# Optimization experiments

Measured on AMD Instinct MI355X. Metric: run time of the kernel, lower is better.

## Reference

```python
import jax, jax.numpy as jnp
import numpy as np

B, T, D, H, LORA = 4, 1024, 1024, 16, 64
HD = D // H
BLOCK_ID, N_BLOCKS = 6, 12


def _ln(x, w, b, eps=1e-5):
    m = x.mean(-1, keepdims=True)
    v = ((x - m) ** 2).mean(-1, keepdims=True)
    return (x - m) * jax.lax.rsqrt(v + eps) * w + b


def _lora(z, a, b, l):
    return l + jnp.tanh(z @ a.T) @ b.T


def setup_inputs() -> dict:
    key = jax.random.key(0)
    ks = iter(jax.random.split(key, 64))
    rn = lambda shape, s: jax.random.normal(next(ks), shape, jnp.float32) * s
    inp = {}
    inp['x'] = rn((B, T, D), 1.0)
    r1 = 1.0 - BLOCK_ID / N_BLOCKS
    i = np.arange(D)
    inp['xw'] = jnp.asarray(1.0 - (i / D) ** r1, jnp.float32)
    for nm in ('rW', 'kW', 'vW', 'gW'):
        inp[nm] = rn((D, D), 0.02)
    for p in ('r', 'k', 'v', 'g', 'd'):
        inp[p + '_la'] = rn((LORA, D), 0.001)
        inp[p + '_lb'] = rn((D, LORA), 0.001)
        inp[p + '_ll'] = rn((D,), 1.0)
    inp['ln_w'] = jnp.full((HD,), ((1 + BLOCK_ID) / N_BLOCKS) ** 0.7, jnp.float32)
    inp['ln_b'] = jnp.zeros((HD,), jnp.float32)
    inp['oW'] = rn((D, D), 0.02)
    inp['init_state'] = rn((H, HD, HD), 1.0)
    r0 = BLOCK_ID / (N_BLOCKS - 1)
    ih = i % HD
    inp['u'] = jnp.asarray(r0 * (1 - ih / (D - 1)) + np.remainder(0.1 * (ih + 1), 3.0), jnp.float32)
    return inp


def reference(x, xw, rW, kW, vW, gW, r_la, r_lb, r_ll, k_la, k_lb, k_ll,
              v_la, v_lb, v_ll, g_la, g_lb, g_ll, d_la, d_lb, d_ll,
              ln_w, ln_b, oW, init_state, u):
    b, t, d = x.shape
    h = init_state.shape[0]
    hd = d // h
    # token shift: xx[t] = x[t-1], xx[0] = 0
    xx = jnp.concatenate([jnp.zeros_like(x[:, :1]), x[:, :-1]], axis=1)
    dx = xx - x
    lerpx = x + dx * xw
    r = (x + dx * _lora(lerpx, r_la, r_lb, r_ll)) @ rW.T
    k = (x + dx * _lora(lerpx, k_la, k_lb, k_ll)) @ kW.T
    v = (x + dx * _lora(lerpx, v_la, v_lb, v_ll)) @ vW.T
    g = (x + dx * _lora(lerpx, g_la, g_lb, g_ll)) @ gW.T
    w = jnp.exp(-jnp.exp(_lora(x + dx * _lora(lerpx, d_la, d_lb, d_ll), d_la, d_lb, d_ll)))
    # [B,T,D] -> [T,B,H,hd] for the time scan
    split = lambda z: z.reshape(b, t, h, hd).transpose(1, 0, 2, 3)
    rs, ws, ks, vs = split(r), split(w), split(k), split(v)
    uh = u.reshape(h, hd)
    st0 = jnp.broadcast_to(init_state, (b, h, hd, hd))

    def step(st, inp):
        rt, wt, kt, vt = inp
        kv = jnp.einsum('bhi,bhj->bhij', kt, vt)      # outer product
        y = jnp.einsum('bhi,bhij->bhj', rt, st + uh[None, :, :, None] * kv)
        return wt[..., None] * st + kv, y             # diag(w) @ S + kv

    st1, ys = jax.lax.scan(step, st0, (rs, ws, ks, vs))  # ys: [T,B,H,hd]
    o = jax.nn.silu(g.reshape(b, t, h, hd)) * _ln(ys.transpose(1, 0, 2, 3), ln_w, ln_b)
    return o.reshape(b, t, d) @ oW.T, st1
```

## Files before the change

### kernel.cpp

```cpp
#include <hip/hip_runtime.h>
#include <hip/hip_bf16.h>

typedef unsigned short u16;
typedef unsigned int u32;
typedef __attribute__((ext_vector_type(4))) float f32x4;
typedef __attribute__((ext_vector_type(4))) u32 u32x4;
typedef __attribute__((ext_vector_type(8))) short s16x8;

#define AS1 __attribute__((address_space(1)))
#define AS3 __attribute__((address_space(3)))

#define NB 4
#define TTOK 1024
#define DD 1024
#define NH 16
#define HD 64
#define MT 4096
#define NCH 16
#define CLEN 64

static __device__ __forceinline__ float b2f(u16 u) {
  union { unsigned int u; float f; } c; c.u = ((unsigned int)u) << 16; return c.f;
}
static __device__ __forceinline__ float ubit(u32 u) {
  union { u32 u; float f; } c; c.u = u; return c.f;
}
static __device__ __forceinline__ u16 f2b(float f) {
  union { float f; unsigned int u; } c; c.f = f;
  return (u16)((c.u + 0x7fffu + ((c.u >> 16) & 1u)) >> 16);
}
static __device__ __forceinline__ void gload16(const u16* g, u16* l) {
  __builtin_amdgcn_global_load_lds((const AS1 u32*)g, (AS3 u32*)l, 16, 0, 0);
}
static __device__ __forceinline__ int swz(int lin) {
  return lin ^ (((lin >> 9) & 3) << 5) ^ (((lin >> 7) & 1) << 4);
}

__global__ __launch_bounds__(256) void convW(const float* __restrict__ s0, const float* __restrict__ s1,
                                             const float* __restrict__ s2, const float* __restrict__ s3,
                                             const float* __restrict__ s4, u16* __restrict__ dst) {
  long f = ((long)blockIdx.x * 256 + threadIdx.x) << 2;
  int sel = (int)(f >> 20);
  const float* s = sel == 0 ? s0 : sel == 1 ? s1 : sel == 2 ? s2 : sel == 3 ? s3 : s4;
  long off = f & 1048575;
  f32x4 v = *(const f32x4*)&s[off];
  ushort4 o; o.x = f2b(v[0]); o.y = f2b(v[1]); o.z = f2b(v[2]); o.w = f2b(v[3]);
  *(ushort4*)&dst[f] = o;
}

__global__ __launch_bounds__(256) void convLora(
    const float* a0, const float* a1, const float* a2, const float* a3, const float* a4,
    const float* b0, const float* b1, const float* b2, const float* b3, const float* b4,
    const float* l0, const float* l1, const float* l2, const float* l3, const float* l4,
    u16* __restrict__ laD, u16* __restrict__ lbD, float* __restrict__ llD) {
  long f = ((long)blockIdx.x * 256 + threadIdx.x) << 2;
  if (f < 327680) {
    int sel = (int)(f >> 16); long off = f & 65535;
    const float* s = sel == 0 ? a0 : sel == 1 ? a1 : sel == 2 ? a2 : sel == 3 ? a3 : a4;
    f32x4 v = *(const f32x4*)&s[off];
    ushort4 o; o.x = f2b(v[0]); o.y = f2b(v[1]); o.z = f2b(v[2]); o.w = f2b(v[3]);
    *(ushort4*)&laD[f] = o;
  } else if (f < 655360) {
    long g = f - 327680;
    int sel = (int)(g >> 16); long off = g & 65535;
    const float* s = sel == 0 ? b0 : sel == 1 ? b1 : sel == 2 ? b2 : sel == 3 ? b3 : b4;
    f32x4 v = *(const f32x4*)&s[off];
    ushort4 o; o.x = f2b(v[0]); o.y = f2b(v[1]); o.z = f2b(v[2]); o.w = f2b(v[3]);
    *(ushort4*)&lbD[g] = o;
  } else if (f < 660480) {
    long g = f - 655360;
    int sel = (int)(g >> 10); long off = g & 1023;
    const float* s = sel == 0 ? l0 : sel == 1 ? l1 : sel == 2 ? l2 : sel == 3 ? l3 : l4;
    *(f32x4*)&llD[g] = *(const f32x4*)&s[off];
  }
}

__global__ __launch_bounds__(256) void prep(const float* __restrict__ x, const float* __restrict__ xw,
                                            u16* __restrict__ lerpx, u16* __restrict__ xB,
                                            u16* __restrict__ dxB) {
  long f = ((long)blockIdx.x * 256 + threadIdx.x) << 2;
  int d = (int)(f & (DD - 1));
  int m = (int)(f >> 10);
  int t = m & (TTOK - 1);
  f32x4 xv = *(const f32x4*)&x[f];
  f32x4 xm = {};
  if (t > 0) xm = *(const f32x4*)&x[f - DD];
  f32x4 xwv = *(const f32x4*)&xw[d];
  f32x4 dx = xm - xv;
  f32x4 lp = xv + dx * xwv;
  ushort4 o; o.x = f2b(lp[0]); o.y = f2b(lp[1]); o.z = f2b(lp[2]); o.w = f2b(lp[3]);
  *(ushort4*)&lerpx[f] = o;
  ushort4 ox; ox.x = f2b(xv[0]); ox.y = f2b(xv[1]); ox.z = f2b(xv[2]); ox.w = f2b(xv[3]);
  *(ushort4*)&xB[f] = ox;
  ushort4 od; od.x = f2b(dx[0]); od.y = f2b(dx[1]); od.z = f2b(dx[2]); od.w = f2b(dx[3]);
  *(ushort4*)&dxB[f] = od;
}

template<int BM, int BN, int EPI>
__launch_bounds__(256)
__global__ void gemm2(const u16* __restrict__ Ab, long sAz,
                      const u16* __restrict__ Bb, long sBz,
                      void* __restrict__ Ob, long sOz,
                      const float* __restrict__ llb,
                      const u16* __restrict__ xB,
                      const u16* __restrict__ dxB,
                      int M, int N, int K) {
  __shared__ __align__(16) u16 As[BM * 64];
  __shared__ __align__(16) u16 Bs[BN * 64];
  const int z = blockIdx.z;
  const u16* A = Ab + (long)z * sAz;
  const u16* Bw = Bb + (long)z * sBz;
  const int m0 = blockIdx.y * BM;
  const int n0 = blockIdx.x * BN;
  const int tid = threadIdx.x;
  const int l = tid & 63;
  const int wv = tid >> 6;
  constexpr int WM = BM / 2, WN = BN / 2;
  constexpr int FM = WM / 16, FN = WN / 16;
  const int wm0 = (wv >> 1) * WM, wn0 = (wv & 1) * WN;
  const int lrow = l & 15, lk = (l >> 4) * 8;
  constexpr int GA = BM / 32, GB = BN / 32;
  int gA[GA], gB[GB];
#pragma unroll
  for (int q = 0; q < GA; ++q) {
    int d = (q * 256 + tid) * 16;
    int bb = swz(d);
    gA[q] = (m0 + (bb >> 7)) * K + ((bb & 127) >> 1);
  }
#pragma unroll
  for (int q = 0; q < GB; ++q) {
    int d = (q * 256 + tid) * 16;
    int bb = swz(d);
    gB[q] = (n0 + (bb >> 7)) * K + ((bb & 127) >> 1);
  }
  int aOff[FM][2], bOff[FN][2];
#pragma unroll
  for (int m = 0; m < FM; ++m)
#pragma unroll
    for (int kk = 0; kk < 2; ++kk)
      aOff[m][kk] = swz(((wm0 + m * 16 + lrow) << 7) + (kk << 6) + (lk << 1));
#pragma unroll
  for (int n = 0; n < FN; ++n)
#pragma unroll
    for (int kk = 0; kk < 2; ++kk)
      bOff[n][kk] = swz(((wn0 + n * 16 + lrow) << 7) + (kk << 6) + (lk << 1));
  f32x4 acc[FM][FN] = {};
  for (int k0 = 0; k0 < K; k0 += 64) {
    __syncthreads();
#pragma unroll
    for (int q = 0; q < GA; ++q)
      gload16(&A[(long)gA[q] + k0], (u16*)((char*)As + (q * 256 + tid) * 16));
#pragma unroll
    for (int q = 0; q < GB; ++q)
      gload16(&Bw[(long)gB[q] + k0], (u16*)((char*)Bs + (q * 256 + tid) * 16));
    __syncthreads();
#pragma unroll
    for (int kk = 0; kk < 2; ++kk) {
      s16x8 af[FM], bfr[FN];
#pragma unroll
      for (int m = 0; m < FM; ++m) af[m] = *(const s16x8*)((const char*)As + aOff[m][kk]);
#pragma unroll
      for (int n = 0; n < FN; ++n) bfr[n] = *(const s16x8*)((const char*)Bs + bOff[n][kk]);
#pragma unroll
      for (int m = 0; m < FM; ++m)
#pragma unroll
        for (int n = 0; n < FN; ++n)
          acc[m][n] = __builtin_amdgcn_mfma_f32_16x16x32_bf16(af[m], bfr[n], acc[m][n], 0, 0, 0);
    }
  }
#pragma unroll
  for (int m = 0; m < FM; ++m) {
#pragma unroll
    for (int n = 0; n < FN; ++n) {
      const int j = n0 + wn0 + n * 16 + lrow;
#pragma unroll
      for (int q = 0; q < 4; ++q) {
        const int i = m0 + wm0 + m * 16 + (l >> 4) * 4 + q;
        const long off = (long)i * N + j;
        float v = acc[m][n][q];
        if constexpr (EPI == 0) {
          ((float*)Ob + (long)z * sOz)[off] = v;
        } else if constexpr (EPI == 1) {
          ((u16*)Ob + (long)z * sOz)[off] = f2b(tanhf(v));
        } else if constexpr (EPI == 2) {
          float val = b2f(xB[off]) + b2f(dxB[off]) * (llb[(long)z * N + j] + v);
          ((u16*)Ob + (long)z * sOz)[off] = f2b(val);
        } else if constexpr (EPI == 3) {
          ((float*)Ob + (long)z * sOz)[off] = expf(-expf(llb[j] + v));
        } else {
          ((u16*)Ob + (long)z * sOz)[off] = f2b(v);
        }
      }
    }
  }
}

__global__ __launch_bounds__(256) void scan_local(
    const u16* __restrict__ rP, const u16* __restrict__ kP,
    const u16* __restrict__ vP, const float* __restrict__ wP,
    const float* __restrict__ uP,
    u16* __restrict__ ys0, u16* __restrict__ ys1,
    u16* __restrict__ ys2, u16* __restrict__ ys3,
    u16* __restrict__ rtil, float* __restrict__ SL, float* __restrict__ AC) {
  __shared__ __align__(16) u16 Rs[64 * 64];
  __shared__ __align__(16) u16 Ks[64 * 64];
  __shared__ __align__(16) u16 Vs[64 * 64];
  __shared__ __align__(16) float Ws[64 * 64];
  const int bhc = blockIdx.x;
  const int c = bhc & (NCH - 1), h = (bhc >> 4) & (NH - 1), b = bhc >> 8;
  const int tid = threadIdx.x;
  const int j = tid & 63;
  const int qu = tid >> 6;
  const long base0 = ((long)(b * TTOK + c * CLEN) << 10) + h * HD;
#pragma unroll
  for (int q = 0; q < 2; ++q) {
    int cidx = q * 256 + tid;
    int t = cidx >> 3, off = (cidx & 7) * 8;
    gload16(&rP[base0 + (long)t * DD + off], (u16*)Rs + cidx * 8);
    gload16(&kP[base0 + (long)t * DD + off], (u16*)Ks + cidx * 8);
    gload16(&vP[base0 + (long)t * DD + off], (u16*)Vs + cidx * 8);
  }
#pragma unroll
  for (int q = 0; q < 4; ++q) {
    int cidx = q * 256 + tid;
    int t = cidx >> 4, off = (cidx & 15) * 4;
    __builtin_amdgcn_global_load_lds((const AS1 u32*)&wP[base0 + (long)t * DD + off],
                                     (AS3 u32*)((float*)Ws + cidx * 4), 16, 0, 0);
  }
  __syncthreads();
  const int so = qu * 16;
  float s[16];
#pragma unroll
  for (int x = 0; x < 16; ++x) s[x] = 0.f;
  float Aj = 1.f;
  const float uj = uP[h * HD + j];
  long base = base0;
  u16* __restrict__ ysel = qu == 0 ? ys0 : qu == 1 ? ys1 : qu == 2 ? ys2 : ys3;
  for (int tt = 0; tt < CLEN; ++tt) {
    const int ro = tt * 64 + so;
    u32x4 ra = *(const u32x4*)&Rs[ro];
    u32x4 rb = *(const u32x4*)&Rs[ro + 8];
    u32x4 ka = *(const u32x4*)&Ks[ro];
    u32x4 kb = *(const u32x4*)&Ks[ro + 8];
    float wl[16];
#pragma unroll
    for (int e = 0; e < 4; ++e) *(f32x4*)&wl[e * 4] = *(const f32x4*)&Ws[ro + e * 4];
    const float vj = b2f(Vs[tt * 64 + j]);
    float ya = 0.f, yb = 0.f;
#pragma unroll
    for (int e = 0; e < 4; ++e) {
      const float r0 = ubit(ra[e] << 16), r1 = ubit(ra[e] & 0xffff0000u);
      const float k0 = ubit(ka[e] << 16), k1 = ubit(ka[e] & 0xffff0000u);
      ya = fmaf(r0, s[2 * e], ya);
      s[2 * e] = fmaf(wl[2 * e], s[2 * e], k0 * vj);
      yb = fmaf(r1, s[2 * e + 1], yb);
      s[2 * e + 1] = fmaf(wl[2 * e + 1], s[2 * e + 1], k1 * vj);
    }
#pragma unroll
    for (int e = 0; e < 4; ++e) {
      const float r0 = ubit(rb[e] << 16), r1 = ubit(rb[e] & 0xffff0000u);
      const float k0 = ubit(kb[e] << 16), k1 = ubit(kb[e] & 0xffff0000u);
      ya = fmaf(r0, s[8 + 2 * e], ya);
      s[8 + 2 * e] = fmaf(wl[8 + 2 * e], s[8 + 2 * e], k0 * vj);
      yb = fmaf(r1, s[8 + 2 * e + 1], yb);
      s[8 + 2 * e + 1] = fmaf(wl[8 + 2 * e + 1], s[8 + 2 * e + 1], k1 * vj);
    }
    float y = ya + yb;
    if (qu == 0) {
      const float rj = b2f(Rs[tt * 64 + j]);
      const float kj = b2f(Ks[tt * 64 + j]);
      const float wj = Ws[tt * 64 + j];
      rtil[base + j] = f2b(rj * Aj);
      float al = rj * uj * kj;
#pragma unroll
      for (int msk = 1; msk < 64; msk <<= 1) al += __shfl_xor(al, msk, 64);
      y = fmaf(al, vj, y);
      Aj *= wj;
    }
    ysel[base + j] = f2b(y);
    base += DD;
  }
#pragma unroll
  for (int x = 0; x < 16; ++x)
    SL[((long)bhc * 64 + so + x) * 64 + j] = s[x];
  if (qu == 0) AC[(long)bhc * 64 + j] = Aj;
}

__global__ __launch_bounds__(256) void scan_prop(
    float* __restrict__ SL, const float* __restrict__ AC,
    const float* __restrict__ initS, float* __restrict__ st1) {
  const int bh = blockIdx.x >> 2;
  const int jq = blockIdx.x & 3;
  const int h = bh & (NH - 1);
  const int i = threadIdx.x >> 2;
  const int jo = jq * 16 + (threadIdx.x & 3) * 4;
  f32x4 sin4 = *(const f32x4*)(initS + ((long)h * 64 + i) * 64 + jo);
  for (int cc = 0; cc < NCH; ++cc) {
    const long bhc = (long)bh * NCH + cc;
    f32x4* slp = (f32x4*)(SL + (bhc * 64 + i) * 64 + jo);
    const float Ai = AC[bhc * 64 + i];
    f32x4 sl = *slp;
    *slp = sin4;
    sin4 = Ai * sin4 + sl;
  }
  *(f32x4*)(st1 + ((long)bh * 64 + i) * 64 + jo) = sin4;
}

__global__ __launch_bounds__(256) void scan_corr(
    const float* __restrict__ SL, const u16* __restrict__ rtil, float* __restrict__ ysC) {
  __shared__ __align__(16) float S[64 * 64];
  const int bhc = blockIdx.x;
  const int c = bhc & (NCH - 1), h = (bhc >> 4) & (NH - 1), b = bhc >> 8;
  const int tid = threadIdx.x;
  const f32x4* sp = (const f32x4*)(SL + (long)bhc * 4096);
  for (int q = tid; q < 1024; q += 256) ((f32x4*)S)[q] = sp[q];
  __syncthreads();
  const int t = tid >> 2, jg = (tid & 3) * 16;
  const long base = ((long)(b * TTOK + c * CLEN + t) * DD) + h * HD;
  f32x4 yacc[4] = {};
  const u16* rp = rtil + base;
#pragma unroll 8
  for (int i = 0; i < 64; ++i) {
    const float r = b2f(rp[i]);
    const f32x4* srow = (const f32x4*)&S[i * 64 + jg];
#pragma unroll
    for (int e = 0; e < 4; ++e) yacc[e] += r * srow[e];
  }
  f32x4* yp = (f32x4*)(ysC + base + jg);
#pragma unroll
  for (int e = 0; e < 4; ++e) yp[e] = yacc[e];
}

__global__ __launch_bounds__(256) void ln_silu(
    const u16* __restrict__ p0, const u16* __restrict__ p1,
    const u16* __restrict__ p2, const u16* __restrict__ p3,
    const float* __restrict__ ysC,
    const u16* __restrict__ gP,
    const float* __restrict__ lnw, const float* __restrict__ lnb,
    u16* __restrict__ oB) {
  const int ridx = blockIdx.x * 4 + (threadIdx.x >> 6);
  const int lane = threadIdx.x & 63;
  const long basem = (long)ridx * 64;
  const float y = b2f(p0[basem + lane]) + b2f(p1[basem + lane]) +
                  b2f(p2[basem + lane]) + b2f(p3[basem + lane]) + ysC[basem + lane];
  float su = y, sq = y * y;
#pragma unroll
  for (int msk = 1; msk < 64; msk <<= 1) {
    su += __shfl_xor(su, msk, 64);
    sq += __shfl_xor(sq, msk, 64);
  }
  const float mean = su * (1.f / 64.f);
  const float var = sq * (1.f / 64.f) - mean * mean;
  const float rs = rsqrtf(var + 1e-5f);
  const float g = b2f(gP[basem + lane]);
  const float silu = g / (1.f + expf(-g));
  const float val = silu * ((y - mean) * rs * lnw[lane] + lnb[lane]);
  oB[basem + lane] = f2b(val);
}

extern "C" void kernel_launch(void* const* d_in, const int* in_sizes, int n_in,
                              void* d_out, int out_size, void* d_ws, size_t ws_size,
                              hipStream_t stream) {
  const float* x   = (const float*)d_in[0];
  const float* xw  = (const float*)d_in[1];
  const float* rW  = (const float*)d_in[2];
  const float* kW  = (const float*)d_in[3];
  const float* vW  = (const float*)d_in[4];
  const float* gW  = (const float*)d_in[5];
  const float* r_la = (const float*)d_in[6],  *r_lb = (const float*)d_in[7],  *r_ll = (const float*)d_in[8];
  const float* k_la = (const float*)d_in[9],  *k_lb = (const float*)d_in[10], *k_ll = (const float*)d_in[11];
  const float* v_la = (const float*)d_in[12], *v_lb = (const float*)d_in[13], *v_ll = (const float*)d_in[14];
  const float* g_la = (const float*)d_in[15], *g_lb = (const float*)d_in[16], *g_ll = (const float*)d_in[17];
  const float* d_la = (const float*)d_in[18], *d_lb = (const float*)d_in[19], *d_ll = (const float*)d_in[20];
  const float* lnw = (const float*)d_in[21];
  const float* lnb = (const float*)d_in[22];
  const float* oW  = (const float*)d_in[23];
  const float* initS = (const float*)d_in[24];
  const float* uP  = (const float*)d_in[25];
  float* out = (float*)d_out;

  char* ws = (char*)d_ws;
  u16*   W_all  = (u16*)(ws + 0);
  u16*   la_all = (u16*)(ws + 10485760);
  u16*   lb_all = (u16*)(ws + 11141120);
  float* ll_all = (float*)(ws + 11796480);
  u16*   lerpx  = (u16*)(ws + 11816960);
  u16*   xB     = (u16*)(ws + 20205568);
  u16*   dxB    = (u16*)(ws + 28594176);
  u16*   t1_all = (u16*)(ws + 36982784);
  u16*   z_all  = (u16*)(ws + 39604224);
  u16*   rkvg   = (u16*)(ws + 81547264);
  float* wbuf   = (float*)(ws + 115101696);
  u16*   rtil   = (u16*)(ws + 131878912);
  float* SL     = (float*)(ws + 140267520);
  float* AC     = (float*)(ws + 157044736);
  u16*   ys0p   = (u16*)(ws + 157306880);
  u16*   oB     = (u16*)(ws + 174084096);
  u16*   ys1p   = (u16*)(ws + 11816960);
  u16*   ys2p   = (u16*)(ws + 39604224);
  u16*   ys3p   = (u16*)(ws + 47992832);
  float* ysC    = (float*)(ws + 115101696);

  convW<<<5120, 256, 0, stream>>>(rW, kW, vW, gW, oW, W_all);
  convLora<<<645, 256, 0, stream>>>(r_la, k_la, v_la, g_la, d_la,
                                    r_lb, k_lb, v_lb, g_lb, d_lb,
                                    r_ll, k_ll, v_ll, g_ll, d_ll,
                                    la_all, lb_all, ll_all);
  prep<<<4096, 256, 0, stream>>>(x, xw, lerpx, xB, dxB);

  gemm2<64, 64, 1><<<dim3(1, 64, 5), 256, 0, stream>>>(
      lerpx, 0L, la_all, 65536L, (void*)t1_all, 262144L, nullptr, nullptr, nullptr, MT, 64, 1024);
  gemm2<128, 128, 2><<<dim3(8, 32, 5), 256, 0, stream>>>(
      t1_all, 262144L, lb_all, 65536L, (void*)z_all, 4194304L, ll_all, xB, dxB, MT, 1024, 64);
  gemm2<64, 64, 1><<<dim3(1, 64, 1), 256, 0, stream>>>(
      z_all + 4L * 4194304, 0L, la_all + 4L * 65536, 0L, (void*)t1_all, 0L, nullptr, nullptr, nullptr, MT, 64, 1024);
  gemm2<128, 128, 3><<<dim3(8, 32, 1), 256, 0, stream>>>(
      t1_all, 0L, lb_all + 4L * 65536, 0L, (void*)wbuf, 0L, ll_all + 4096, nullptr, nullptr, MT, 1024, 64);
  gemm2<128, 128, 4><<<dim3(8, 32, 4), 256, 0, stream>>>(
      z_all, 4194304L, W_all, 1048576L, (void*)rkvg, 4194304L, nullptr, nullptr, nullptr, MT, 1024, 1024);

  scan_local<<<1024, 256, 0, stream>>>(rkvg, rkvg + 4194304L, rkvg + 2L * 4194304, wbuf,
                                       uP, ys0p, ys1p, ys2p, ys3p, rtil, SL, AC);
  scan_prop<<<256, 256, 0, stream>>>(SL, AC, initS, out + 4194304);
  scan_corr<<<1024, 256, 0, stream>>>(SL, rtil, ysC);

  ln_silu<<<16384, 256, 0, stream>>>(ys0p, ys1p, ys2p, ys3p, ysC, rkvg + 3L * 4194304, lnw, lnb, oB);
  gemm2<128, 128, 0><<<dim3(8, 32, 1), 256, 0, stream>>>(
      oB, 0L, W_all + 4L * 1048576, 0L, (void*)out, 0L, nullptr, nullptr, nullptr, MT, 1024, 1024);
}
```

Measured before the change: 368.4 us.

## Split scan state rows across 8 waves with packed FMA and swap GEMM grid order

The chunk-local scan now runs 512 threads per block, so each wave holds 8 state rows instead of 16. Its inner loop uses two-wide float vector FMAs, and the rtil and bonus-term work moves onto two different waves. Partial y outputs grow from four buffers to eight, and ln_silu sums all eight. GEMM block indexing is also swapped so the M tiles vary along blockIdx.x, which changes tile scheduling order. Serial per-block latency should fall, at the cost of more partial-output traffic and extra workspace aliasing.

```diff
diff --git a/kernel.cpp b/kernel.cpp
--- a/kernel.cpp
+++ b/kernel.cpp
@@ -3,6 +3,7 @@
 
 typedef unsigned short u16;
 typedef unsigned int u32;
+typedef __attribute__((ext_vector_type(2))) float f32x2;
 typedef __attribute__((ext_vector_type(4))) float f32x4;
 typedef __attribute__((ext_vector_type(4))) u32 u32x4;
 typedef __attribute__((ext_vector_type(8))) short s16x8;
@@ -18,6 +19,9 @@
 #define MT 4096
 #define NCH 16
 #define CLEN 64
+
+struct Ptr8 { u16* p[8]; };
+struct CPtr8 { const u16* p[8]; };
 
 static __device__ __forceinline__ float b2f(u16 u) {
   union { unsigned int u; float f; } c; c.u = ((unsigned int)u) << 16; return c.f;
@@ -110,8 +114,8 @@
   const int z = blockIdx.z;
   const u16* A = Ab + (long)z * sAz;
   const u16* Bw = Bb + (long)z * sBz;
-  const int m0 = blockIdx.y * BM;
-  const int n0 = blockIdx.x * BN;
+  const int m0 = blockIdx.x * BM;
+  const int n0 = blockIdx.y * BN;
   const int tid = threadIdx.x;
   const int l = tid & 63;
   const int wv = tid >> 6;
@@ -195,12 +199,10 @@
   }
 }
 
-__global__ __launch_bounds__(256) void scan_local(
+__global__ __launch_bounds__(512) void scan_local(
     const u16* __restrict__ rP, const u16* __restrict__ kP,
     const u16* __restrict__ vP, const float* __restrict__ wP,
-    const float* __restrict__ uP,
-    u16* __restrict__ ys0, u16* __restrict__ ys1,
-    u16* __restrict__ ys2, u16* __restrict__ ys3,
+    const float* __restrict__ uP, Ptr8 YS,
     u16* __restrict__ rtil, float* __restrict__ SL, float* __restrict__ AC) {
   __shared__ __align__(16) u16 Rs[64 * 64];
   __shared__ __align__(16) u16 Ks[64 * 64];
@@ -212,77 +214,68 @@
   const int j = tid & 63;
   const int qu = tid >> 6;
   const long base0 = ((long)(b * TTOK + c * CLEN) << 10) + h * HD;
+  {
+    int t = tid >> 3, off = (tid & 7) * 8;
+    gload16(&rP[base0 + (long)t * DD + off], (u16*)Rs + tid * 8);
+    gload16(&kP[base0 + (long)t * DD + off], (u16*)Ks + tid * 8);
+    gload16(&vP[base0 + (long)t * DD + off], (u16*)Vs + tid * 8);
+  }
 #pragma unroll
   for (int q = 0; q < 2; ++q) {
-    int cidx = q * 256 + tid;
-    int t = cidx >> 3, off = (cidx & 7) * 8;
-    gload16(&rP[base0 + (long)t * DD + off], (u16*)Rs + cidx * 8);
-    gload16(&kP[base0 + (long)t * DD + off], (u16*)Ks + cidx * 8);
-    gload16(&vP[base0 + (long)t * DD + off], (u16*)Vs + cidx * 8);
-  }
-#pragma unroll
-  for (int q = 0; q < 4; ++q) {
-    int cidx = q * 256 + tid;
+    int cidx = q * 512 + tid;
     int t = cidx >> 4, off = (cidx & 15) * 4;
     __builtin_amdgcn_global_load_lds((const AS1 u32*)&wP[base0 + (long)t * DD + off],
                                      (AS3 u32*)((float*)Ws + cidx * 4), 16, 0, 0);
   }
   __syncthreads();
-  const int so = qu * 16;
-  float s[16];
-#pragma unroll
-  for (int x = 0; x < 16; ++x) s[x] = 0.f;
+  const int so = qu * 8;
+  f32x2 s2[4] = {};
   float Aj = 1.f;
-  const float uj = uP[h * HD + j];
+  const float uj = (qu == 1) ? uP[h * HD + j] : 0.f;
   long base = base0;
-  u16* __restrict__ ysel = qu == 0 ? ys0 : qu == 1 ? ys1 : qu == 2 ? ys2 : ys3;
+  u16* __restrict__ ysel =
+      qu == 0 ? YS.p[0] : qu == 1 ? YS.p[1] : qu == 2 ? YS.p[2] : qu == 3 ? YS.p[3] :
+      qu == 4 ? YS.p[4] : qu == 5 ? YS.p[5] : qu == 6 ? YS.p[6] : YS.p[7];
   for (int tt = 0; tt < CLEN; ++tt) {
     const int ro = tt * 64 + so;
     u32x4 ra = *(const u32x4*)&Rs[ro];
-    u32x4 rb = *(const u32x4*)&Rs[ro + 8];
     u32x4 ka = *(const u32x4*)&Ks[ro];
-    u32x4 kb = *(const u32x4*)&Ks[ro + 8];
-    float wl[16];
-#pragma unroll
-    for (int e = 0; e < 4; ++e) *(f32x4*)&wl[e * 4] = *(const f32x4*)&Ws[ro + e * 4];
+    f32x2 wv2[4];
+#pragma unroll
+    for (int e = 0; e < 4; ++e) wv2[e] = *(const f32x2*)&Ws[ro + 2 * e];
     const float vj = b2f(Vs[tt * 64 + j]);
-    float ya = 0.f, yb = 0.f;
+    const f32x2 vj2 = {vj, vj};
+    f32x2 y2 = {0.f, 0.f};
 #pragma unroll
     for (int e = 0; e < 4; ++e) {
-      const float r0 = ubit(ra[e] << 16), r1 = ubit(ra[e] & 0xffff0000u);
-      const float k0 = ubit(ka[e] << 16), k1 = ubit(ka[e] & 0xffff0000u);
-      ya = fmaf(r0, s[2 * e], ya);
-      s[2 * e] = fmaf(wl[2 * e], s[2 * e], k0 * vj);
-      yb = fmaf(r1, s[2 * e + 1], yb);
-      s[2 * e + 1] = fmaf(wl[2 * e + 1], s[2 * e + 1], k1 * vj);
+      const u32 pr = ra[e], pk = ka[e];
+      f32x2 r01; r01[0] = ubit(pr << 16); r01[1] = ubit(pr & 0xffff0000u);
+      f32x2 k01; k01[0] = ubit(pk << 16); k01[1] = ubit(pk & 0xffff0000u);
+      y2 = __builtin_elementwise_fma(r01, s2[e], y2);
+      s2[e] = __builtin_elementwise_fma(wv2[e], s2[e], k01 * vj2);
     }
-#pragma unroll
-    for (int e = 0; e < 4; ++e) {
-      const float r0 = ubit(rb[e] << 16), r1 = ubit(rb[e] & 0xffff0000u);
-      const float k0 = ubit(kb[e] << 16), k1 = ubit(kb[e] & 0xffff0000u);
-      ya = fmaf(r0, s[8 + 2 * e], ya);
-      s[8 + 2 * e] = fmaf(wl[8 + 2 * e], s[8 + 2 * e], k0 * vj);
-      yb = fmaf(r1, s[8 + 2 * e + 1], yb);
-      s[8 + 2 * e + 1] = fmaf(wl[8 + 2 * e + 1], s[8 + 2 * e + 1], k1 * vj);
-    }
-    float y = ya + yb;
+    float y = y2[0] + y2[1];
     if (qu == 0) {
       const float rj = b2f(Rs[tt * 64 + j]);
-      const float kj = b2f(Ks[tt * 64 + j]);
       const float wj = Ws[tt * 64 + j];
       rtil[base + j] = f2b(rj * Aj);
+      Aj *= wj;
+    } else if (qu == 1) {
+      const float rj = b2f(Rs[tt * 64 + j]);
+      const float kj = b2f(Ks[tt * 64 + j]);
       float al = rj * uj * kj;
 #pragma unroll
       for (int msk = 1; msk < 64; msk <<= 1) al += __shfl_xor(al, msk, 64);
       y = fmaf(al, vj, y);
-      Aj *= wj;
     }
     ysel[base + j] = f2b(y);
     base += DD;
   }
 #pragma unroll
-  for (int x = 0; x < 16; ++x)
-    SL[((long)bhc * 64 + so + x) * 64 + j] = s[x];
+  for (int e = 0; e < 4; ++e) {
+    SL[((long)bhc * 64 + so + 2 * e) * 64 + j] = s2[e][0];
+    SL[((long)bhc * 64 + so + 2 * e + 1) * 64 + j] = s2[e][1];
+  }
   if (qu == 0) AC[(long)bhc * 64 + j] = Aj;
 }
 
@@ -332,17 +325,16 @@
 }
 
 __global__ __launch_bounds__(256) void ln_silu(
-    const u16* __restrict__ p0, const u16* __restrict__ p1,
-    const u16* __restrict__ p2, const u16* __restrict__ p3,
-    const float* __restrict__ ysC,
+    CPtr8 P, const float* __restrict__ ysC,
     const u16* __restrict__ gP,
     const float* __restrict__ lnw, const float* __restrict__ lnb,
     u16* __restrict__ oB) {
   const int ridx = blockIdx.x * 4 + (threadIdx.x >> 6);
   const int lane = threadIdx.x & 63;
   const long basem = (long)ridx * 64;
-  const float y = b2f(p0[basem + lane]) + b2f(p1[basem + lane]) +
-                  b2f(p2[basem + lane]) + b2f(p3[basem + lane]) + ysC[basem + lane];
+  float y = ysC[basem + lane];
+#pragma unroll
+  for (int q = 0; q < 8; ++q) y += b2f(P.p[q][basem + lane]);
   float su = y, sq = y * y;
 #pragma unroll
   for (int msk = 1; msk < 64; msk <<= 1) {
@@ -396,10 +388,17 @@
   float* AC     = (float*)(ws + 157044736);
   u16*   ys0p   = (u16*)(ws + 157306880);
   u16*   oB     = (u16*)(ws + 174084096);
-  u16*   ys1p   = (u16*)(ws + 11816960);
-  u16*   ys2p   = (u16*)(ws + 39604224);
-  u16*   ys3p   = (u16*)(ws + 47992832);
   float* ysC    = (float*)(ws + 115101696);
+
+  Ptr8 YS;
+  YS.p[0] = ys0p;
+  YS.p[1] = (u16*)(ws + 11816960);
+  YS.p[2] = (u16*)(ws + 20205568);
+  YS.p[3] = (u16*)(ws + 28594176);
+  YS.p[4] = (u16*)(ws + 39604224);
+  YS.p[5] = (u16*)(ws + 47992832);
+  YS.p[6] = (u16*)(ws + 56381440);
+  YS.p[7] = (u16*)(ws + 64770048);
 
   convW<<<5120, 256, 0, stream>>>(rW, kW, vW, gW, oW, W_all);
   convLora<<<645, 256, 0, stream>>>(r_la, k_la, v_la, g_la, d_la,
@@ -408,23 +407,25 @@
                                     la_all, lb_all, ll_all);
   prep<<<4096, 256, 0, stream>>>(x, xw, lerpx, xB, dxB);
 
-  gemm2<64, 64, 1><<<dim3(1, 64, 5), 256, 0, stream>>>(
+  gemm2<64, 64, 1><<<dim3(64, 1, 5), 256, 0, stream>>>(
       lerpx, 0L, la_all, 65536L, (void*)t1_all, 262144L, nullptr, nullptr, nullptr, MT, 64, 1024);
-  gemm2<128, 128, 2><<<dim3(8, 32, 5), 256, 0, stream>>>(
+  gemm2<128, 128, 2><<<dim3(32, 8, 5), 256, 0, stream>>>(
       t1_all, 262144L, lb_all, 65536L, (void*)z_all, 4194304L, ll_all, xB, dxB, MT, 1024, 64);
-  gemm2<64, 64, 1><<<dim3(1, 64, 1), 256, 0, stream>>>(
+  gemm2<64, 64, 1><<<dim3(64, 1, 1), 256, 0, stream>>>(
       z_all + 4L * 4194304, 0L, la_all + 4L * 65536, 0L, (void*)t1_all, 0L, nullptr, nullptr, nullptr, MT, 64, 1024);
-  gemm2<128, 128, 3><<<dim3(8, 32, 1), 256, 0, stream>>>(
+  gemm2<128, 128, 3><<<dim3(32, 8, 1), 256, 0, stream>>>(
       t1_all, 0L, lb_all + 4L * 65536, 0L, (void*)wbuf, 0L, ll_all + 4096, nullptr, nullptr, MT, 1024, 64);
-  gemm2<128, 128, 4><<<dim3(8, 32, 4), 256, 0, stream>>>(
+  gemm2<128, 128, 4><<<dim3(32, 8, 4), 256, 0, stream>>>(
       z_all, 4194304L, W_all, 1048576L, (void*)rkvg, 4194304L, nullptr, nullptr, nullptr, MT, 1024, 1024);
 
-  scan_local<<<1024, 256, 0, stream>>>(rkvg, rkvg + 4194304L, rkvg + 2L * 4194304, wbuf,
-                                       uP, ys0p, ys1p, ys2p, ys3p, rtil, SL, AC);
+  scan_local<<<1024, 512, 0, stream>>>(rkvg, rkvg + 4194304L, rkvg + 2L * 4194304, wbuf,
+                                       uP, YS, rtil, SL, AC);
   scan_prop<<<256, 256, 0, stream>>>(SL, AC, initS, out + 4194304);
   scan_corr<<<1024, 256, 0, stream>>>(SL, rtil, ysC);
 
-  ln_silu<<<16384, 256, 0, stream>>>(ys0p, ys1p, ys2p, ys3p, ysC, rkvg + 3L * 4194304, lnw, lnb, oB);
-  gemm2<128, 128, 0><<<dim3(8, 32, 1), 256, 0, stream>>>(
+  CPtr8 YSc;
+  for (int q = 0; q < 8; ++q) YSc.p[q] = YS.p[q];
+  ln_silu<<<16384, 256, 0, stream>>>(YSc, ysC, rkvg + 3L * 4194304, lnw, lnb, oB);
+  gemm2<128, 128, 0><<<dim3(32, 8, 1), 256, 0, stream>>>(
       oB, 0L, W_all + 4L * 1048576, 0L, (void*)out, 0L, nullptr, nullptr, nullptr, MT, 1024, 1024);
 }
```

After: 352.4 us. 1.05x faster.
